# Performance work log

Hardware: AMD Instinct MI355X
Metric: run time of the kernel (lower is better)

The kernel has to match this reference:

```python
import jax, jax.numpy as jnp
import numpy as np

N_BATCH, N_JOINTS, FEAT = 4096, 52, 256  # N_batch = B*T, SMPL-X-like joint count
LN_EPS = 1e-5


def setup_inputs() -> dict:
    key = jax.random.key(0)
    k0, k1, k2 = jax.random.split(key, 3)
    x = jax.random.normal(k0, (N_BATCH, N_JOINTS, FEAT), dtype=jnp.float32)

    # Kinematic tree as a chain: parent of joint i+1 is joint i.
    parents = np.arange(N_JOINTS - 1, dtype=np.int32)
    children = np.arange(1, N_JOINTS, dtype=np.int32)
    src = np.concatenate([parents, children])   # parent->child then child->parent
    dst = np.concatenate([children, parents])
    edge_index = jnp.asarray(np.stack([src, dst]), dtype=jnp.int32)  # (2, E)
    edge_type = jnp.concatenate([
        jnp.zeros(N_JOINTS - 1, dtype=jnp.int32),
        jnp.ones(N_JOINTS - 1, dtype=jnp.int32),
    ])  # (E,)

    # Two edge-type message linears, stacked (torch Linear weight layout: [out, in]).
    W = jax.random.normal(k1, (2, FEAT, FEAT), dtype=jnp.float32) / np.sqrt(FEAT)
    pose_emb = jax.random.normal(k2, (N_JOINTS, FEAT), dtype=jnp.float32)
    ln_gamma = jnp.ones((FEAT,), dtype=jnp.float32)
    ln_beta = jnp.zeros((FEAT,), dtype=jnp.float32)
    return {
        "x": x,
        "W": W,
        "pose_emb": pose_emb,
        "ln_gamma": ln_gamma,
        "ln_beta": ln_beta,
        "edge_index": edge_index,
        "edge_type": edge_type,
    }


def reference(x, W, pose_emb, ln_gamma, ln_beta, edge_index, edge_type):
    # x: (B, N, C); edge_index: (2, E); edge_type: (E,); W: (n_types, C, C)
    src = edge_index[0]
    dst = edge_index[1]
    diff = x[:, src, :] - x[:, dst, :]                # (B, E, C) gathered difference
    # Per-edge anisotropic linear: select weight by edge type, msg = diff @ W_et^T
    msg = jnp.einsum("bei,eoi->beo", diff, W[edge_type])  # (B, E, C)
    agg = jnp.zeros_like(x).at[:, dst, :].add(msg)    # scatter-add over destination joint
    agg = agg + pose_emb[None, :, :]                  # pose embedding per joint
    h = x + jax.nn.gelu(agg, approximate=False)       # torch GELU default is exact (erf)
    mu = jnp.mean(h, axis=-1, keepdims=True)
    var = jnp.mean(jnp.square(h - mu), axis=-1, keepdims=True)
    return (h - mu) * jax.lax.rsqrt(var + LN_EPS) * ln_gamma + ln_beta
```

## Files before the change

kernel.cpp:

```cpp
#include <hip/hip_runtime.h>
#include <hip/hip_bf16.h>
#include <math.h>


#define NB   4096
#define NJ   52
#define FEAT 256
#define M_TOT (NB * NJ)
#define BM   128
#define NKT  8

typedef float  f32x4  __attribute__((ext_vector_type(4)));
typedef short  bf16x8 __attribute__((ext_vector_type(8)));
typedef unsigned short u16;

__device__ __forceinline__ u16 f2bf(float f) {
  unsigned u = __builtin_bit_cast(unsigned, f);
  u += 0x7FFFu + ((u >> 16) & 1u);
  return (u16)(u >> 16);
}

typedef __attribute__((address_space(1))) const unsigned int as1c_u32;
typedef __attribute__((address_space(3))) unsigned int       as3_u32;
__device__ __forceinline__ void g2lds16(const void* g, void* l) {
  __builtin_amdgcn_global_load_lds((as1c_u32*)g, (as3_u32*)l, 16, 0, 0);
}

__global__ void KinGNN_wprep(const float* __restrict__ W, u16* __restrict__ Wp) {
  const int o = blockIdx.x;
  const int k = threadIdx.x;
  const float v = W[((k >> 8) << 16) + o * FEAT + (k & 255)];
  Wp[(o << 9) + k] = f2bf(v);
}

__global__ __launch_bounds__(512, 4) void KinGNN_fused(
    const float* __restrict__ x, const u16* __restrict__ Wp,
    const float* __restrict__ pose, const float* __restrict__ gamma,
    const float* __restrict__ beta, float* __restrict__ out) {
  __shared__ __align__(16) unsigned char smem[49152];
  unsigned char* Asb = smem;
  unsigned char* Bsb = smem + 16384;
  float* red = (float*)smem;

  const int tid  = threadIdx.x;
  const int lane = tid & 63;
  const int w    = tid >> 6;
  const int wr   = w >> 2;
  const int wc   = w & 3;
  const int l15  = lane & 15;
  const int lg   = lane >> 4;
  const int m0   = blockIdx.x * BM;

  f32x4 acc[4][4];
  #pragma unroll
  for (int i = 0; i < 4; ++i)
    #pragma unroll
    for (int j = 0; j < 4; ++j) {
      f32x4 z = {0.f, 0.f, 0.f, 0.f};
      acc[i][j] = z;
    }

  const int ar  = tid >> 2;
  const int am  = m0 + ar;
  const int aj  = am % NJ;
  const int akb = (tid & 3) * 32;
  const int swzA = (ar & 7) << 4;
  unsigned char* awp0 = Asb + ((ar * 128 + akb) ^ swzA);
  unsigned char* awp1 = Asb + ((ar * 128 + akb + 16) ^ swzA);

  for (int kt = 0; kt < NKT; ++kt) {
    {
      const int half = kt >> 2;
      const int kx = (kt & 3) * 64 + (akb >> 1);
      const bool valid = half ? (aj <= NJ - 2) : (aj >= 1);
      const float* xc = x + (size_t)am * FEAT + kx;
      const float* xn = valid ? (half ? xc + FEAT : xc - FEAT) : xc;
      f32x4 c0 = *(const f32x4*)(xc + 0),  c1 = *(const f32x4*)(xc + 4);
      f32x4 c2 = *(const f32x4*)(xc + 8),  c3 = *(const f32x4*)(xc + 12);
      f32x4 n0 = *(const f32x4*)(xn + 0),  n1 = *(const f32x4*)(xn + 4);
      f32x4 n2 = *(const f32x4*)(xn + 8),  n3 = *(const f32x4*)(xn + 12);
      float d[16];
      #pragma unroll
      for (int e = 0; e < 4; ++e) {
        d[e]      = valid ? (n0[e] - c0[e]) : 0.f;
        d[e + 4]  = valid ? (n1[e] - c1[e]) : 0.f;
        d[e + 8]  = valid ? (n2[e] - c2[e]) : 0.f;
        d[e + 12] = valid ? (n3[e] - c3[e]) : 0.f;
      }
      bf16x8 p0, p1;
      #pragma unroll
      for (int e = 0; e < 8; ++e) {
        p0[e] = (short)f2bf(d[e]);
        p1[e] = (short)f2bf(d[e + 8]);
      }
      *(bf16x8*)awp0 = p0;
      *(bf16x8*)awp1 = p1;
    }
    {
      const unsigned char* Wb = (const unsigned char*)Wp;
      #pragma unroll
      for (int i = 0; i < 4; ++i) {
        const int p   = (w * 4 + i) * 1024 + lane * 16;
        const int row = p >> 7;
        const int off = p & 127;
        const void* g = Wb + row * 1024 + kt * 128 + (off ^ ((row & 7) << 4));
        g2lds16(g, Bsb + (w * 4 + i) * 1024);
      }
    }
    __syncthreads();
    #pragma unroll
    for (int kf = 0; kf < 2; ++kf) {
      const int kb = kf * 64 + lg * 16;
      bf16x8 a[4];
      #pragma unroll
      for (int mf = 0; mf < 4; ++mf) {
        const int r = wr * 64 + mf * 16 + l15;
        a[mf] = *(const bf16x8*)(Asb + ((r * 128 + kb) ^ ((r & 7) << 4)));
      }
      #pragma unroll
      for (int nf = 0; nf < 4; ++nf) {
        const int o = wc * 64 + nf * 16 + l15;
        bf16x8 b = *(const bf16x8*)(Bsb + ((o * 128 + kb) ^ ((o & 7) << 4)));
        #pragma unroll
        for (int mf = 0; mf < 4; ++mf)
          acc[mf][nf] = __builtin_amdgcn_mfma_f32_16x16x32_bf16(a[mf], b, acc[mf][nf], 0, 0, 0);
      }
    }
    __syncthreads();
  }

  float gm[4], bt[4];
  #pragma unroll
  for (int nf = 0; nf < 4; ++nf) {
    const int col = wc * 64 + nf * 16 + l15;
    gm[nf] = gamma[col];
    bt[nf] = beta[col];
  }
  float s[4][4], ss[4][4];
  #pragma unroll
  for (int mf = 0; mf < 4; ++mf) {
    #pragma unroll
    for (int rg = 0; rg < 4; ++rg) {
      const int r = m0 + wr * 64 + mf * 16 + lg * 4 + rg;
      const int j = r % NJ;
      float su = 0.f, sq = 0.f;
      #pragma unroll
      for (int nf = 0; nf < 4; ++nf) {
        const int col = wc * 64 + nf * 16 + l15;
        float a = acc[mf][nf][rg] + pose[j * FEAT + col];
        float g = 0.5f * a * (1.0f + erff(a * 0.70710678118654752f));
        float h = x[(size_t)r * FEAT + col] + g;
        acc[mf][nf][rg] = h;
        su += h;
        sq += h * h;
      }
      #pragma unroll
      for (int dd = 1; dd < 16; dd <<= 1) {
        su += __shfl_xor(su, dd);
        sq += __shfl_xor(sq, dd);
      }
      s[mf][rg] = su;
      ss[mf][rg] = sq;
    }
  }
  if (l15 == 0) {
    #pragma unroll
    for (int mf = 0; mf < 4; ++mf)
      #pragma unroll
      for (int rg = 0; rg < 4; ++rg) {
        const int rl = wr * 64 + mf * 16 + lg * 4 + rg;
        red[(wc * 128 + rl) * 2 + 0] = s[mf][rg];
        red[(wc * 128 + rl) * 2 + 1] = ss[mf][rg];
      }
  }
  __syncthreads();
  #pragma unroll
  for (int mf = 0; mf < 4; ++mf) {
    #pragma unroll
    for (int rg = 0; rg < 4; ++rg) {
      const int rl = wr * 64 + mf * 16 + lg * 4 + rg;
      float S = 0.f, SS = 0.f;
      #pragma unroll
      for (int q = 0; q < 4; ++q) {
        S  += red[(q * 128 + rl) * 2 + 0];
        SS += red[(q * 128 + rl) * 2 + 1];
      }
      const float mu   = S * (1.0f / 256.0f);
      const float var  = SS * (1.0f / 256.0f) - mu * mu;
      const float rstd = rsqrtf(var + 1e-5f);
      const int r = m0 + wr * 64 + mf * 16 + lg * 4 + rg;
      #pragma unroll
      for (int nf = 0; nf < 4; ++nf) {
        const int col = wc * 64 + nf * 16 + l15;
        out[(size_t)r * FEAT + col] = (acc[mf][nf][rg] - mu) * rstd * gm[nf] + bt[nf];
      }
    }
  }
}

extern "C" void kernel_launch(void* const* d_in, const int* in_sizes, int n_in,
                              void* d_out, int out_size, void* d_ws, size_t ws_size,
                              hipStream_t stream) {
  const float* x     = (const float*)d_in[0];
  const float* W     = (const float*)d_in[1];
  const float* pose  = (const float*)d_in[2];
  const float* gamma = (const float*)d_in[3];
  const float* beta  = (const float*)d_in[4];
  u16* Wp = (u16*)d_ws;

  KinGNN_wprep<<<dim3(FEAT), dim3(512), 0, stream>>>(W, Wp);
  KinGNN_fused<<<dim3(M_TOT / BM), dim3(512), 0, stream>>>(x, Wp, pose, gamma, beta,
                                                           (float*)d_out);
}
```

Baseline: 613.0 us.

## Stage fp32 x tile with halo in LDS once, compute diffs from LDS, fast erf

Instead of each thread loading current and neighbour rows from global memory for every k-tile, the kernel stages a 130-row fp32 x slab (with halo rows) into LDS via async global_load_lds. The edge differences and their bf16 conversion are computed from LDS while building the MFMA A fragments. The weight tiles are restaged per half, so each x chunk is read once from global memory for both edge directions. Exact erff is replaced with the Abramowitz-Stegun polynomial approximation. LDS use grows to about 66KB, which likely cuts occupancy, and the erf approximation adds small numerical error.

After: 821.6 us. 1.34x slower.

```diff
diff --git a/kernel.cpp b/kernel.cpp
--- a/kernel.cpp
+++ b/kernel.cpp
@@ -8,7 +8,6 @@
 #define FEAT 256
 #define M_TOT (NB * NJ)
 #define BM   128
-#define NKT  8
 
 typedef float  f32x4  __attribute__((ext_vector_type(4)));
 typedef short  bf16x8 __attribute__((ext_vector_type(8)));
@@ -24,6 +23,18 @@
 typedef __attribute__((address_space(3))) unsigned int       as3_u32;
 __device__ __forceinline__ void g2lds16(const void* g, void* l) {
   __builtin_amdgcn_global_load_lds((as1c_u32*)g, (as3_u32*)l, 16, 0, 0);
+}
+
+__device__ __forceinline__ float erf_fast(float xx) {
+  const float ax = fabsf(xx);
+  const float t  = 1.0f / (1.0f + 0.3275911f * ax);
+  const float y  = t * (0.254829592f +
+                   t * (-0.284496736f +
+                   t * (1.421413741f +
+                   t * (-1.453152027f +
+                   t * 1.061405429f))));
+  const float r = 1.0f - y * __expf(-ax * ax);
+  return xx < 0.0f ? -r : r;
 }
 
 __global__ void KinGNN_wprep(const float* __restrict__ W, u16* __restrict__ Wp) {
@@ -37,9 +48,9 @@
     const float* __restrict__ x, const u16* __restrict__ Wp,
     const float* __restrict__ pose, const float* __restrict__ gamma,
     const float* __restrict__ beta, float* __restrict__ out) {
-  __shared__ __align__(16) unsigned char smem[49152];
-  unsigned char* Asb = smem;
-  unsigned char* Bsb = smem + 16384;
+  extern __shared__ __align__(16) unsigned char smem[];
+  unsigned char* Xs  = smem;
+  unsigned char* Bsb = smem + 33280;
   float* red = (float*)smem;
 
   const int tid  = threadIdx.x;
@@ -60,73 +71,88 @@
       acc[i][j] = z;
     }
 
-  const int ar  = tid >> 2;
-  const int am  = m0 + ar;
-  const int aj  = am % NJ;
-  const int akb = (tid & 3) * 32;
-  const int swzA = (ar & 7) << 4;
-  unsigned char* awp0 = Asb + ((ar * 128 + akb) ^ swzA);
-  unsigned char* awp1 = Asb + ((ar * 128 + akb + 16) ^ swzA);
-
-  for (int kt = 0; kt < NKT; ++kt) {
-    {
-      const int half = kt >> 2;
-      const int kx = (kt & 3) * 64 + (akb >> 1);
-      const bool valid = half ? (aj <= NJ - 2) : (aj >= 1);
-      const float* xc = x + (size_t)am * FEAT + kx;
-      const float* xn = valid ? (half ? xc + FEAT : xc - FEAT) : xc;
-      f32x4 c0 = *(const f32x4*)(xc + 0),  c1 = *(const f32x4*)(xc + 4);
-      f32x4 c2 = *(const f32x4*)(xc + 8),  c3 = *(const f32x4*)(xc + 12);
-      f32x4 n0 = *(const f32x4*)(xn + 0),  n1 = *(const f32x4*)(xn + 4);
-      f32x4 n2 = *(const f32x4*)(xn + 8),  n3 = *(const f32x4*)(xn + 12);
-      float d[16];
-      #pragma unroll
-      for (int e = 0; e < 4; ++e) {
-        d[e]      = valid ? (n0[e] - c0[e]) : 0.f;
-        d[e + 4]  = valid ? (n1[e] - c1[e]) : 0.f;
-        d[e + 8]  = valid ? (n2[e] - c2[e]) : 0.f;
-        d[e + 12] = valid ? (n3[e] - c3[e]) : 0.f;
-      }
-      bf16x8 p0, p1;
-      #pragma unroll
-      for (int e = 0; e < 8; ++e) {
-        p0[e] = (short)f2bf(d[e]);
-        p1[e] = (short)f2bf(d[e + 8]);
-      }
-      *(bf16x8*)awp0 = p0;
-      *(bf16x8*)awp1 = p1;
-    }
-    {
-      const unsigned char* Wb = (const unsigned char*)Wp;
-      #pragma unroll
-      for (int i = 0; i < 4; ++i) {
-        const int p   = (w * 4 + i) * 1024 + lane * 16;
-        const int row = p >> 7;
-        const int off = p & 127;
-        const void* g = Wb + row * 1024 + kt * 128 + (off ^ ((row & 7) << 4));
-        g2lds16(g, Bsb + (w * 4 + i) * 1024);
-      }
-    }
+  bool v0[4], v1[4];
+  #pragma unroll
+  for (int mf = 0; mf < 4; ++mf) {
+    const int gr = m0 + wr * 64 + mf * 16 + l15;
+    const int aj = gr % NJ;
+    v0[mf] = (aj >= 1);
+    v1[mf] = (aj <= NJ - 2);
+  }
+
+  auto stageX = [&](int s) {
+    #pragma unroll
+    for (int i = 0; i < 4; ++i) {
+      const int p   = (i * 512 + tid) * 16 + 256;
+      const int row = p >> 8;
+      const int off = p & 255;
+      const char* g = (const char*)x + (size_t)(m0 - 1 + row) * 1024 + s * 256
+                      + (off ^ ((row & 7) << 4));
+      g2lds16(g, Xs + p);
+    }
+    if (tid < 32) {
+      const int hi  = tid >> 4, l = tid & 15;
+      const int row = hi ? 129 : 0;
+      const int gr2 = hi ? (m0 + 128 < M_TOT ? m0 + 128 : M_TOT - 1)
+                         : (m0 - 1 >= 0 ? m0 - 1 : 0);
+      f32x4 v = *(const f32x4*)((const char*)x + (size_t)gr2 * 1024 + s * 256 + l * 16);
+      *(f32x4*)(Xs + ((row * 256 + l * 16) ^ ((row & 7) << 4))) = v;
+    }
+  };
+  auto stageB = [&](int s, int h) {
+    #pragma unroll
+    for (int i = 0; i < 4; ++i) {
+      const int p   = (i * 512 + tid) * 16;
+      const int q   = p >> 7;
+      const int off = p & 127;
+      const char* g = (const char*)Wp + q * 1024 + h * 512 + s * 128
+                      + (off ^ ((q & 7) << 4));
+      g2lds16(g, Bsb + p);
+    }
+  };
+
+  stageX(0);
+  stageB(0, 0);
+
+  for (int kt = 0; kt < 8; ++kt) {
+    const int s = kt >> 1, h = kt & 1;
     __syncthreads();
     #pragma unroll
     for (int kf = 0; kf < 2; ++kf) {
-      const int kb = kf * 64 + lg * 16;
       bf16x8 a[4];
       #pragma unroll
       for (int mf = 0; mf < 4; ++mf) {
-        const int r = wr * 64 + mf * 16 + l15;
-        a[mf] = *(const bf16x8*)(Asb + ((r * 128 + kb) ^ ((r & 7) << 4)));
+        const int ci   = wr * 64 + mf * 16 + l15 + 1;
+        const int ni   = h ? ci + 1 : ci - 1;
+        const int off  = kf * 128 + lg * 32;
+        const int cswz = (ci & 7) << 4, nswz = (ni & 7) << 4;
+        const f32x4 cA = *(const f32x4*)(Xs + ((ci * 256 + off) ^ cswz));
+        const f32x4 cB = *(const f32x4*)(Xs + ((ci * 256 + off + 16) ^ cswz));
+        const f32x4 nA = *(const f32x4*)(Xs + ((ni * 256 + off) ^ nswz));
+        const f32x4 nB = *(const f32x4*)(Xs + ((ni * 256 + off + 16) ^ nswz));
+        bf16x8 fr;
+        #pragma unroll
+        for (int e = 0; e < 4; ++e) {
+          fr[e]     = (short)f2bf(nA[e] - cA[e]);
+          fr[e + 4] = (short)f2bf(nB[e] - cB[e]);
+        }
+        const bf16x8 zr = {0, 0, 0, 0, 0, 0, 0, 0};
+        a[mf] = (h ? v1[mf] : v0[mf]) ? fr : zr;
       }
       #pragma unroll
       for (int nf = 0; nf < 4; ++nf) {
-        const int o = wc * 64 + nf * 16 + l15;
-        bf16x8 b = *(const bf16x8*)(Bsb + ((o * 128 + kb) ^ ((o & 7) << 4)));
+        const int q = wc * 64 + nf * 16 + l15;
+        bf16x8 b = *(const bf16x8*)(Bsb + ((q * 128 + kf * 64 + lg * 16) ^ ((q & 7) << 4)));
         #pragma unroll
         for (int mf = 0; mf < 4; ++mf)
           acc[mf][nf] = __builtin_amdgcn_mfma_f32_16x16x32_bf16(a[mf], b, acc[mf][nf], 0, 0, 0);
       }
     }
     __syncthreads();
+    if (kt < 7) {
+      stageB(s + h, h ^ 1);
+      if (h) stageX(s + 1);
+    }
   }
 
   float gm[4], bt[4];
@@ -136,7 +162,7 @@
     gm[nf] = gamma[col];
     bt[nf] = beta[col];
   }
-  float s[4][4], ss[4][4];
+  float s_[4][4], ss[4][4];
   #pragma unroll
   for (int mf = 0; mf < 4; ++mf) {
     #pragma unroll
@@ -147,19 +173,19 @@
       #pragma unroll
       for (int nf = 0; nf < 4; ++nf) {
         const int col = wc * 64 + nf * 16 + l15;
-        float a = acc[mf][nf][rg] + pose[j * FEAT + col];
-        float g = 0.5f * a * (1.0f + erff(a * 0.70710678118654752f));
-        float h = x[(size_t)r * FEAT + col] + g;
-        acc[mf][nf][rg] = h;
-        su += h;
-        sq += h * h;
+        float av = acc[mf][nf][rg] + pose[j * FEAT + col];
+        float g  = 0.5f * av * (1.0f + erf_fast(av * 0.70710678118654752f));
+        float hv = x[(size_t)r * FEAT + col] + g;
+        acc[mf][nf][rg] = hv;
+        su += hv;
+        sq += hv * hv;
       }
       #pragma unroll
       for (int dd = 1; dd < 16; dd <<= 1) {
         su += __shfl_xor(su, dd);
         sq += __shfl_xor(sq, dd);
       }
-      s[mf][rg] = su;
+      s_[mf][rg] = su;
       ss[mf][rg] = sq;
     }
   }
@@ -169,7 +195,7 @@
       #pragma unroll
       for (int rg = 0; rg < 4; ++rg) {
         const int rl = wr * 64 + mf * 16 + lg * 4 + rg;
-        red[(wc * 128 + rl) * 2 + 0] = s[mf][rg];
+        red[(wc * 128 + rl) * 2 + 0] = s_[mf][rg];
         red[(wc * 128 + rl) * 2 + 1] = ss[mf][rg];
       }
   }
@@ -208,7 +234,12 @@
   const float* beta  = (const float*)d_in[4];
   u16* Wp = (u16*)d_ws;
 
+  static int lds_attr_set = 0;
+  (void)hipFuncSetAttribute((const void*)KinGNN_fused,
+                            hipFuncAttributeMaxDynamicSharedMemorySize, 66048);
+  (void)lds_attr_set;
+
   KinGNN_wprep<<<dim3(FEAT), dim3(512), 0, stream>>>(W, Wp);
-  KinGNN_fused<<<dim3(M_TOT / BM), dim3(512), 0, stream>>>(x, Wp, pose, gamma, beta,
-                                                           (float*)d_out);
-}
+  KinGNN_fused<<<dim3(M_TOT / BM), dim3(512), 66048, stream>>>(x, Wp, pose, gamma, beta,
+                                                               (float*)d_out);
+}
```
